# Kernel optimization log

Measured on AMD Instinct MI355X. Metric: run time of the kernel, lower is better.

Reference implementation:

```python
import jax, jax.numpy as jnp
import numpy as np

B, N = 4096, 512


def setup_inputs() -> dict:
    key = jax.random.key(0)
    ks = jax.random.split(key, 8)
    waypoints = jax.random.normal(ks[0], (B, N, 2), dtype=jnp.float32)
    # learned params: scalar smooth_weight + curvature_net MLP (4->64->32->1)
    smooth_weight = jnp.float32(0.3)
    W1 = jax.random.normal(ks[1], (4, 64), dtype=jnp.float32) * 0.5
    b1 = jnp.zeros((64,), dtype=jnp.float32)
    W2 = jax.random.normal(ks[2], (64, 32), dtype=jnp.float32) * 0.125
    b2 = jnp.zeros((32,), dtype=jnp.float32)
    W3 = jax.random.normal(ks[3], (32, 1), dtype=jnp.float32) * 0.18
    b3 = jnp.zeros((1,), dtype=jnp.float32)
    return {"waypoints": waypoints, "smooth_weight": smooth_weight,
            "W1": W1, "b1": b1, "W2": W2, "b2": b2, "W3": W3, "b3": b3}


def _forward(waypoints, smooth_weight, W1, b1, W2, b2, W3, b3):
    Bq, Nq, _ = waypoints.shape
    # finite differences
    d1 = waypoints[:, 1:] - waypoints[:, :-1]          # (B, N-1, 2)
    d2 = d1[:, 1:] - d1[:, :-1]                        # (B, N-2, 2)
    d1 = jnp.concatenate([d1, d1[:, -1:]], axis=1)     # (B, N, 2)
    z = jnp.zeros((Bq, 1, 2), dtype=waypoints.dtype)
    d2 = jnp.concatenate([z, d2, z], axis=1)           # (B, N, 2)
    feats = jnp.concatenate([d1, d2], axis=-1)         # (B, N, 4)
    # curvature MLP -> sigmoid weight in (0,1)
    h = jax.nn.relu(jnp.einsum('bnf,fh->bnh', feats, W1) + b1)
    h = jax.nn.relu(jnp.einsum('bnh,hk->bnk', h, W2) + b2)
    cw = jax.nn.sigmoid(jnp.einsum('bnk,ko->bno', h, W3) + b3)  # (B, N, 1)
    sw = jax.nn.sigmoid(smooth_weight)
    w = sw * (1.0 - cw[..., 0])                        # (B, N)
    # linear recurrence: y_i = w_i * y_{i-1} + (1-w_i) * x_i, y_0 = x_0
    a = jnp.swapaxes(w[:, 1:], 0, 1)                   # (N-1, B)
    x = jnp.swapaxes(waypoints[:, 1:], 0, 1)           # (N-1, B, 2)

    def step(carry, inp):
        a_i, x_i = inp
        y = a_i[:, None] * carry + (1.0 - a_i)[:, None] * x_i
        return y, y

    _, ys = jax.lax.scan(step, waypoints[:, 0], (a, x))
    smoothed = jnp.concatenate([waypoints[:, :1], jnp.swapaxes(ys, 0, 1)], axis=1)
    # endpoints pinned to original (start already equals input)
    smoothed = smoothed.at[:, -1].set(waypoints[:, -1])
    return smoothed


def reference(waypoints, smooth_weight, W1, b1, W2, b2, W3, b3):
    return _forward(waypoints, smooth_weight, W1, b1, W2, b2, W3, b3)
```

## Files before the change

kernel.cpp:

```cpp
#include <hip/hip_runtime.h>
#include <math.h>

#define NPT 512
#define BROWS 4096
#define TAB_U4 17

typedef _Float16 half8 __attribute__((ext_vector_type(8)));
typedef _Float16 h2    __attribute__((ext_vector_type(2)));
typedef float    f32x4 __attribute__((ext_vector_type(4)));
typedef unsigned int u32x4 __attribute__((ext_vector_type(4)));

__device__ __forceinline__ float sigmoidf_fast(float x) {
    return 1.0f / (1.0f + __expf(-x));
}

__device__ __forceinline__ h2 pkrtz(float a, float b) {
    return __builtin_bit_cast(h2, __builtin_amdgcn_cvt_pkrtz(a, b));
}

#if __has_builtin(__builtin_amdgcn_fdot2)
__device__ __forceinline__ float fdot2(h2 a, h2 b, float c) {
    return __builtin_amdgcn_fdot2(__builtin_bit_cast(__fp16 __attribute__((ext_vector_type(2))), a),
                                  __builtin_bit_cast(__fp16 __attribute__((ext_vector_type(2))), b),
                                  c, false);
}
#else
__device__ __forceinline__ float fdot2(h2 a, h2 b, float c) {
    c = fmaf((float)a[0], (float)b[0], c);
    c = fmaf((float)a[1], (float)b[1], c);
    return c;
}
#endif

__global__ __launch_bounds__(64) void setup_kernel(
    const float* __restrict__ W1, const float* __restrict__ b1,
    const float* __restrict__ W2, const float* __restrict__ b2,
    const float* __restrict__ W3, u32x4* __restrict__ tab)
{
    const int lane = threadIdx.x & 63;
    const int nn   = lane & 15;
    const int kg   = lane >> 4;
    const int kg8  = kg * 8;

    half8 Wf00, Wf01, Wf10, Wf11;
    #pragma unroll
    for (int j = 0; j < 8; ++j) {
        Wf00[j] = (_Float16)W2[(0  + kg8 + j) * 32 + 0  + nn];
        Wf01[j] = (_Float16)W2[(0  + kg8 + j) * 32 + 16 + nn];
        Wf10[j] = (_Float16)W2[(32 + kg8 + j) * 32 + 0  + nn];
        Wf11[j] = (_Float16)W2[(32 + kg8 + j) * 32 + 16 + nn];
    }
    tab[0 * 64 + lane] = __builtin_bit_cast(u32x4, Wf00);
    tab[1 * 64 + lane] = __builtin_bit_cast(u32x4, Wf01);
    tab[2 * 64 + lane] = __builtin_bit_cast(u32x4, Wf10);
    tab[3 * 64 + lane] = __builtin_bit_cast(u32x4, Wf11);

    unsigned int wbuf[32], bbuf[8];
    #pragma unroll
    for (int i = 0; i < 8; ++i) {
        const int ch = (i < 4) ? (kg8 + 2 * i) : (32 + kg8 + 2 * (i - 4));
        #pragma unroll
        for (int k = 0; k < 4; ++k) {
            h2 v; v[0] = (_Float16)W1[k * 64 + ch]; v[1] = (_Float16)W1[k * 64 + ch + 1];
            wbuf[k * 8 + i] = __builtin_bit_cast(unsigned int, v);
        }
        h2 bv; bv[0] = (_Float16)b1[ch]; bv[1] = (_Float16)b1[ch + 1];
        bbuf[i] = __builtin_bit_cast(unsigned int, bv);
    }
    #pragma unroll
    for (int p = 0; p < 8; ++p) {
        u32x4 v;
        v[0] = wbuf[p * 4 + 0]; v[1] = wbuf[p * 4 + 1];
        v[2] = wbuf[p * 4 + 2]; v[3] = wbuf[p * 4 + 3];
        tab[(4 + p) * 64 + lane] = v;
    }
    {
        u32x4 v0, v1;
        #pragma unroll
        for (int e = 0; e < 4; ++e) { v0[e] = bbuf[e]; v1[e] = bbuf[4 + e]; }
        tab[12 * 64 + lane] = v0;
        tab[13 * 64 + lane] = v1;
    }
    f32x4 ai0, ai1;
    u32x4 w3v;
    #pragma unroll
    for (int q = 0; q < 4; ++q) {
        const int ch = kg * 4 + q;
        ai0[q] = b2[ch];
        ai1[q] = b2[16 + ch];
    }
    #pragma unroll
    for (int e = 0; e < 2; ++e) {
        h2 a, b;
        a[0] = (_Float16)W3[kg * 4 + 2 * e];
        a[1] = (_Float16)W3[kg * 4 + 2 * e + 1];
        b[0] = (_Float16)W3[16 + kg * 4 + 2 * e];
        b[1] = (_Float16)W3[16 + kg * 4 + 2 * e + 1];
        w3v[e]     = __builtin_bit_cast(unsigned int, a);
        w3v[2 + e] = __builtin_bit_cast(unsigned int, b);
    }
    tab[14 * 64 + lane] = __builtin_bit_cast(u32x4, ai0);
    tab[15 * 64 + lane] = __builtin_bit_cast(u32x4, ai1);
    tab[16 * 64 + lane] = w3v;
}

__global__ __launch_bounds__(256, 4) void wps_kernel(
    const float* __restrict__ wp,
    const float* __restrict__ sww,
    const float* __restrict__ b3,
    const u32x4* __restrict__ tab,
    float* __restrict__ out)
{
    __shared__ float sLg[2][NPT];
    __shared__ float2 sY[2];

    const int t    = threadIdx.x;
    const int lane = t & 63;
    const int wv   = t >> 6;
    const int row0 = blockIdx.x * 2;

    const int nn = lane & 15;
    const int kg = lane >> 4;

    const half8 Wf00 = __builtin_bit_cast(half8, tab[0 * 64 + lane]);
    const half8 Wf01 = __builtin_bit_cast(half8, tab[1 * 64 + lane]);
    const half8 Wf10 = __builtin_bit_cast(half8, tab[2 * 64 + lane]);
    const half8 Wf11 = __builtin_bit_cast(half8, tab[3 * 64 + lane]);

    h2 w1pk[4][8];
    #pragma unroll
    for (int p = 0; p < 8; ++p) {
        u32x4 v = tab[(4 + p) * 64 + lane];
        #pragma unroll
        for (int e = 0; e < 4; ++e) {
            const int j = p * 4 + e;
            w1pk[j >> 3][j & 7] = __builtin_bit_cast(h2, (unsigned int)v[e]);
        }
    }
    h2 b1pk[8];
    {
        u32x4 v0 = tab[12 * 64 + lane];
        u32x4 v1 = tab[13 * 64 + lane];
        #pragma unroll
        for (int e = 0; e < 4; ++e) {
            b1pk[e]     = __builtin_bit_cast(h2, (unsigned int)v0[e]);
            b1pk[4 + e] = __builtin_bit_cast(h2, (unsigned int)v1[e]);
        }
    }
    const f32x4 accInit0 = __builtin_bit_cast(f32x4, tab[14 * 64 + lane]);
    const f32x4 accInit1 = __builtin_bit_cast(f32x4, tab[15 * 64 + lane]);
    h2 w3p[4];
    {
        u32x4 v = tab[16 * 64 + lane];
        #pragma unroll
        for (int e = 0; e < 4; ++e)
            w3p[e] = __builtin_bit_cast(h2, (unsigned int)v[e]);
    }

    const int seg = wv * 128;

    #pragma unroll
    for (int r = 0; r < 2; ++r) {
        const float2* P = (const float2*)(wp + (size_t)(row0 + r) * NPT * 2);

        #pragma unroll
        for (int s = 0; s < 2; ++s) {
            const int base = seg + s * 64;
            const int g    = base + lane;

            float2 p  = P[g];
            float2 pm = P[(g > 0) ? g - 1 : 0];
            float2 pp = P[(g < NPT - 1) ? g + 1 : NPT - 1];
            float d1x, d1y;
            if (g < NPT - 1) { d1x = pp.x - p.x; d1y = pp.y - p.y; }
            else             { d1x = p.x - pm.x; d1y = p.y - pm.y; }
            float d2x = 0.f, d2y = 0.f;
            if (g >= 1 && g <= NPT - 2) {
                d2x = pp.x - 2.f * p.x + pm.x;
                d2y = pp.y - 2.f * p.y + pm.y;
            }
            h2 f01 = pkrtz(d1x, d1y);
            h2 f23 = pkrtz(d2x, d2y);
            const int u01 = __builtin_bit_cast(int, f01);
            const int u23 = __builtin_bit_cast(int, f23);

            float vkeep = 0.f;

            #pragma unroll
            for (int q = 0; q < 4; ++q) {
                h2 r01 = __builtin_bit_cast(h2, __shfl(u01, q * 16 + nn));
                h2 r23 = __builtin_bit_cast(h2, __shfl(u23, q * 16 + nn));
                h2 f0; f0[0] = f0[1] = r01[0];
                h2 f1; f1[0] = f1[1] = r01[1];
                h2 f2; f2[0] = f2[1] = r23[0];
                h2 f3; f3[0] = f3[1] = r23[1];

                union { half8 v; h2 p[4]; } H0, H1;
                #pragma unroll
                for (int i = 0; i < 8; ++i) {
                    h2 h = b1pk[i];
                    h += f0 * w1pk[0][i];
                    h += f1 * w1pk[1][i];
                    h += f2 * w1pk[2][i];
                    h += f3 * w1pk[3][i];
                    h2 z; z[0] = (_Float16)0.f; z[1] = (_Float16)0.f;
                    h = __builtin_elementwise_max(h, z);
                    if (i < 4) H0.p[i] = h; else H1.p[i - 4] = h;
                }

                f32x4 acc0 = accInit0;
                f32x4 acc1 = accInit1;
                acc0 = __builtin_amdgcn_mfma_f32_16x16x32_f16(Wf00, H0.v, acc0, 0, 0, 0);
                acc0 = __builtin_amdgcn_mfma_f32_16x16x32_f16(Wf10, H1.v, acc0, 0, 0, 0);
                acc1 = __builtin_amdgcn_mfma_f32_16x16x32_f16(Wf01, H0.v, acc1, 0, 0, 0);
                acc1 = __builtin_amdgcn_mfma_f32_16x16x32_f16(Wf11, H1.v, acc1, 0, 0, 0);

                h2 zz; zz[0] = (_Float16)0.f; zz[1] = (_Float16)0.f;
                h2 p0 = __builtin_elementwise_max(pkrtz(acc0[0], acc0[1]), zz);
                h2 p1 = __builtin_elementwise_max(pkrtz(acc0[2], acc0[3]), zz);
                h2 p2 = __builtin_elementwise_max(pkrtz(acc1[0], acc1[1]), zz);
                h2 p3 = __builtin_elementwise_max(pkrtz(acc1[2], acc1[3]), zz);
                float v = fdot2(p0, w3p[0], 0.f);
                v = fdot2(p1, w3p[1], v);
                v = fdot2(p2, w3p[2], v);
                v = fdot2(p3, w3p[3], v);
                v += __shfl_xor(v, 16);
                v += __shfl_xor(v, 32);
                vkeep = (q == kg) ? v : vkeep;
            }

            sLg[r][g] = vkeep;
        }
    }

    __syncthreads();

    {
        const int rloc = wv >> 1;
        const int half = wv & 1;
        const int row  = row0 + rloc;
        const float2* P = (const float2*)(wp + (size_t)row * NPT * 2);
        const float bias3 = b3[0];
        const float swv   = sigmoidf_fast(sww[0]);

        const int base = half * 256 + lane * 4;
        float wr[4];
        *reinterpret_cast<float4*>(&wr[0]) =
            *reinterpret_cast<const float4*>(&sLg[rloc][base]);

        const float4* P4 = (const float4*)P;
        float2 pts[4];
        #pragma unroll
        for (int s = 0; s < 2; ++s) {
            float4 v = P4[base / 2 + s];
            pts[2 * s].x     = v.x; pts[2 * s].y     = v.y;
            pts[2 * s + 1].x = v.z; pts[2 * s + 1].y = v.w;
        }

        float a4[4], cx4[4], cy4[4];
        float A = 1.f, Cx = 0.f, Cy = 0.f;
        #pragma unroll
        for (int i = 0; i < 4; ++i) {
            const int g = base + i;
            float a = (g == 0) ? 0.f
                               : swv * (1.f - sigmoidf_fast(wr[i] + bias3));
            float cx = (1.f - a) * pts[i].x;
            float cy = (1.f - a) * pts[i].y;
            a4[i] = a; cx4[i] = cx; cy4[i] = cy;
            Cx = fmaf(a, Cx, cx);
            Cy = fmaf(a, Cy, cy);
            A *= a;
        }
        #pragma unroll
        for (int d = 1; d < 64; d <<= 1) {
            float Ap  = __shfl_up(A, d);
            float Cpx = __shfl_up(Cx, d);
            float Cpy = __shfl_up(Cy, d);
            if (lane >= d) {
                Cx = fmaf(A, Cpx, Cx);
                Cy = fmaf(A, Cpy, Cy);
                A *= Ap;
            }
        }
        float Aex  = __shfl_up(A, 1);
        float Cxex = __shfl_up(Cx, 1);
        float Cyex = __shfl_up(Cy, 1);

        float4* orow = (float4*)(out + (size_t)row * NPT * 2);

        if (half == 0) {
            float yx = (lane == 0) ? 0.f : Cxex;
            float yy = (lane == 0) ? 0.f : Cyex;
            float ox[4], oy[4];
            #pragma unroll
            for (int i = 0; i < 4; ++i) {
                yx = fmaf(a4[i], yx, cx4[i]);
                yy = fmaf(a4[i], yy, cy4[i]);
                ox[i] = yx; oy[i] = yy;
            }
            orow[base / 2]     = make_float4(ox[0], oy[0], ox[1], oy[1]);
            orow[base / 2 + 1] = make_float4(ox[2], oy[2], ox[3], oy[3]);
            if (lane == 63) { sY[rloc].x = yx; sY[rloc].y = yy; }
        }

        __syncthreads();

        if (half == 1) {
            const float2 y255 = sY[rloc];
            float yx = (lane == 0) ? y255.x : fmaf(Aex, y255.x, Cxex);
            float yy = (lane == 0) ? y255.y : fmaf(Aex, y255.y, Cyex);
            float ox[4], oy[4];
            #pragma unroll
            for (int i = 0; i < 4; ++i) {
                yx = fmaf(a4[i], yx, cx4[i]);
                yy = fmaf(a4[i], yy, cy4[i]);
                ox[i] = yx; oy[i] = yy;
            }
            if (lane == 63) {
                float2 pe = P[NPT - 1];
                ox[3] = pe.x; oy[3] = pe.y;
            }
            orow[base / 2]     = make_float4(ox[0], oy[0], ox[1], oy[1]);
            orow[base / 2 + 1] = make_float4(ox[2], oy[2], ox[3], oy[3]);
        }
    }
}

extern "C" void kernel_launch(void* const* d_in, const int* in_sizes, int n_in,
                              void* d_out, int out_size, void* d_ws, size_t ws_size,
                              hipStream_t stream) {
    const float* wp  = (const float*)d_in[0];
    const float* sww = (const float*)d_in[1];
    const float* W1  = (const float*)d_in[2];
    const float* b1  = (const float*)d_in[3];
    const float* W2  = (const float*)d_in[4];
    const float* b2  = (const float*)d_in[5];
    const float* W3  = (const float*)d_in[6];
    const float* b3  = (const float*)d_in[7];
    float* out = (float*)d_out;
    u32x4* tab = (u32x4*)d_ws;

    setup_kernel<<<1, 64, 0, stream>>>(W1, b1, W2, b2, W3, tab);
    wps_kernel<<<BROWS / 2, 256, 0, stream>>>(wp, sww, b3, tab, out);
}
```

Before: 33.18 us.

## Compute first MLP layer with MFMA instead of packed-half VALU

Moves the 4->64 first layer (with bias folded in through a ones row) from packed fp16 VALU FMAs onto 16x16x16 MFMA instructions. The second layer is restructured into eight 16x16x16 MFMAs whose output layout feeds directly from layer one, so no cross-lane shuffle is needed between layers, and the weight table shrinks from 17 to 9 entries. This trades VALU work and per-lane weight registers for more MFMA issues and extra fmax/convert work on the layer-one outputs, and most of the padded K dimension of layer one is zeros.

```diff
diff --git a/kernel.cpp b/kernel.cpp
--- a/kernel.cpp
+++ b/kernel.cpp
@@ -3,9 +3,10 @@
 
 #define NPT 512
 #define BROWS 4096
-#define TAB_U4 17
+#define TAB_U4 9
 
 typedef _Float16 half8 __attribute__((ext_vector_type(8)));
+typedef _Float16 half4 __attribute__((ext_vector_type(4)));
 typedef _Float16 h2    __attribute__((ext_vector_type(2)));
 typedef float    f32x4 __attribute__((ext_vector_type(4)));
 typedef unsigned int u32x4 __attribute__((ext_vector_type(4)));
@@ -31,6 +32,22 @@
     return c;
 }
 #endif
+
+#if __has_builtin(__builtin_amdgcn_mfma_f32_16x16x16f16)
+__device__ __forceinline__ f32x4 mfma16(half4 a, half4 b, f32x4 c) {
+    return __builtin_amdgcn_mfma_f32_16x16x16f16(a, b, c, 0, 0, 0);
+}
+#else
+__device__ __forceinline__ f32x4 mfma16(half4 a, half4 b, f32x4 c) {
+    half8 a8 = {a[0], a[1], a[2], a[3],
+                (_Float16)0.f, (_Float16)0.f, (_Float16)0.f, (_Float16)0.f};
+    half8 b8 = {b[0], b[1], b[2], b[3],
+                (_Float16)0.f, (_Float16)0.f, (_Float16)0.f, (_Float16)0.f};
+    return __builtin_amdgcn_mfma_f32_16x16x32_f16(a8, b8, c, 0, 0, 0);
+}
+#endif
+
+union H4 { half4 v; h2 p[2]; unsigned int w[2]; };
 
 __global__ __launch_bounds__(64) void setup_kernel(
     const float* __restrict__ W1, const float* __restrict__ b1,
@@ -40,55 +57,63 @@
     const int lane = threadIdx.x & 63;
     const int nn   = lane & 15;
     const int kg   = lane >> 4;
-    const int kg8  = kg * 8;
-
-    half8 Wf00, Wf01, Wf10, Wf11;
-    #pragma unroll
-    for (int j = 0; j < 8; ++j) {
-        Wf00[j] = (_Float16)W2[(0  + kg8 + j) * 32 + 0  + nn];
-        Wf01[j] = (_Float16)W2[(0  + kg8 + j) * 32 + 16 + nn];
-        Wf10[j] = (_Float16)W2[(32 + kg8 + j) * 32 + 0  + nn];
-        Wf11[j] = (_Float16)W2[(32 + kg8 + j) * 32 + 16 + nn];
-    }
-    tab[0 * 64 + lane] = __builtin_bit_cast(u32x4, Wf00);
-    tab[1 * 64 + lane] = __builtin_bit_cast(u32x4, Wf01);
-    tab[2 * 64 + lane] = __builtin_bit_cast(u32x4, Wf10);
-    tab[3 * 64 + lane] = __builtin_bit_cast(u32x4, Wf11);
-
-    unsigned int wbuf[32], bbuf[8];
-    #pragma unroll
-    for (int i = 0; i < 8; ++i) {
-        const int ch = (i < 4) ? (kg8 + 2 * i) : (32 + kg8 + 2 * (i - 4));
-        #pragma unroll
-        for (int k = 0; k < 4; ++k) {
-            h2 v; v[0] = (_Float16)W1[k * 64 + ch]; v[1] = (_Float16)W1[k * 64 + ch + 1];
-            wbuf[k * 8 + i] = __builtin_bit_cast(unsigned int, v);
-        }
-        h2 bv; bv[0] = (_Float16)b1[ch]; bv[1] = (_Float16)b1[ch + 1];
-        bbuf[i] = __builtin_bit_cast(unsigned int, bv);
-    }
-    #pragma unroll
-    for (int p = 0; p < 8; ++p) {
-        u32x4 v;
-        v[0] = wbuf[p * 4 + 0]; v[1] = wbuf[p * 4 + 1];
-        v[2] = wbuf[p * 4 + 2]; v[3] = wbuf[p * 4 + 3];
-        tab[(4 + p) * 64 + lane] = v;
+
+    unsigned int a1w[8];
+    #pragma unroll
+    for (int t = 0; t < 4; ++t) {
+        const int ch = t * 16 + nn;
+        h2 j01, j23;
+        j01[0] = (_Float16)0.f; j01[1] = (_Float16)0.f;
+        j23[0] = (_Float16)0.f; j23[1] = (_Float16)0.f;
+        if (kg == 0) {
+            j01[0] = (_Float16)W1[0 * 64 + ch]; j01[1] = (_Float16)W1[1 * 64 + ch];
+            j23[0] = (_Float16)W1[2 * 64 + ch]; j23[1] = (_Float16)W1[3 * 64 + ch];
+        } else if (kg == 1) {
+            j01[0] = (_Float16)b1[ch];
+        }
+        a1w[t * 2 + 0] = __builtin_bit_cast(unsigned int, j01);
+        a1w[t * 2 + 1] = __builtin_bit_cast(unsigned int, j23);
     }
     {
         u32x4 v0, v1;
         #pragma unroll
-        for (int e = 0; e < 4; ++e) { v0[e] = bbuf[e]; v1[e] = bbuf[4 + e]; }
-        tab[12 * 64 + lane] = v0;
-        tab[13 * 64 + lane] = v1;
-    }
+        for (int e = 0; e < 4; ++e) { v0[e] = a1w[e]; v1[e] = a1w[4 + e]; }
+        tab[0 * 64 + lane] = v0;
+        tab[1 * 64 + lane] = v1;
+    }
+
+    #pragma unroll
+    for (int m = 0; m < 2; ++m) {
+        unsigned int a2w[8];
+        #pragma unroll
+        for (int s = 0; s < 4; ++s) {
+            const int bc  = s * 16 + kg * 4;
+            const int col = m * 16 + nn;
+            h2 j01, j23;
+            j01[0] = (_Float16)W2[(bc + 0) * 32 + col];
+            j01[1] = (_Float16)W2[(bc + 1) * 32 + col];
+            j23[0] = (_Float16)W2[(bc + 2) * 32 + col];
+            j23[1] = (_Float16)W2[(bc + 3) * 32 + col];
+            a2w[s * 2 + 0] = __builtin_bit_cast(unsigned int, j01);
+            a2w[s * 2 + 1] = __builtin_bit_cast(unsigned int, j23);
+        }
+        u32x4 v0, v1;
+        #pragma unroll
+        for (int e = 0; e < 4; ++e) { v0[e] = a2w[e]; v1[e] = a2w[4 + e]; }
+        tab[(2 + m * 2) * 64 + lane] = v0;
+        tab[(3 + m * 2) * 64 + lane] = v1;
+    }
+
     f32x4 ai0, ai1;
+    #pragma unroll
+    for (int r = 0; r < 4; ++r) {
+        ai0[r] = b2[kg * 4 + r];
+        ai1[r] = b2[16 + kg * 4 + r];
+    }
+    tab[6 * 64 + lane] = __builtin_bit_cast(u32x4, ai0);
+    tab[7 * 64 + lane] = __builtin_bit_cast(u32x4, ai1);
+
     u32x4 w3v;
-    #pragma unroll
-    for (int q = 0; q < 4; ++q) {
-        const int ch = kg * 4 + q;
-        ai0[q] = b2[ch];
-        ai1[q] = b2[16 + ch];
-    }
     #pragma unroll
     for (int e = 0; e < 2; ++e) {
         h2 a, b;
@@ -99,9 +124,7 @@
         w3v[e]     = __builtin_bit_cast(unsigned int, a);
         w3v[2 + e] = __builtin_bit_cast(unsigned int, b);
     }
-    tab[14 * 64 + lane] = __builtin_bit_cast(u32x4, ai0);
-    tab[15 * 64 + lane] = __builtin_bit_cast(u32x4, ai1);
-    tab[16 * 64 + lane] = w3v;
+    tab[8 * 64 + lane] = w3v;
 }
 
 __global__ __launch_bounds__(256, 4) void wps_kernel(
@@ -122,40 +145,43 @@
     const int nn = lane & 15;
     const int kg = lane >> 4;
 
-    const half8 Wf00 = __builtin_bit_cast(half8, tab[0 * 64 + lane]);
-    const half8 Wf01 = __builtin_bit_cast(half8, tab[1 * 64 + lane]);
-    const half8 Wf10 = __builtin_bit_cast(half8, tab[2 * 64 + lane]);
-    const half8 Wf11 = __builtin_bit_cast(half8, tab[3 * 64 + lane]);
-
-    h2 w1pk[4][8];
-    #pragma unroll
-    for (int p = 0; p < 8; ++p) {
-        u32x4 v = tab[(4 + p) * 64 + lane];
-        #pragma unroll
-        for (int e = 0; e < 4; ++e) {
-            const int j = p * 4 + e;
-            w1pk[j >> 3][j & 7] = __builtin_bit_cast(h2, (unsigned int)v[e]);
-        }
-    }
-    h2 b1pk[8];
-    {
-        u32x4 v0 = tab[12 * 64 + lane];
-        u32x4 v1 = tab[13 * 64 + lane];
-        #pragma unroll
-        for (int e = 0; e < 4; ++e) {
-            b1pk[e]     = __builtin_bit_cast(h2, (unsigned int)v0[e]);
-            b1pk[4 + e] = __builtin_bit_cast(h2, (unsigned int)v1[e]);
-        }
-    }
-    const f32x4 accInit0 = __builtin_bit_cast(f32x4, tab[14 * 64 + lane]);
-    const f32x4 accInit1 = __builtin_bit_cast(f32x4, tab[15 * 64 + lane]);
+    H4 A1[4];
+    {
+        u32x4 v0 = tab[0 * 64 + lane];
+        u32x4 v1 = tab[1 * 64 + lane];
+        A1[0].w[0] = v0[0]; A1[0].w[1] = v0[1];
+        A1[1].w[0] = v0[2]; A1[1].w[1] = v0[3];
+        A1[2].w[0] = v1[0]; A1[2].w[1] = v1[1];
+        A1[3].w[0] = v1[2]; A1[3].w[1] = v1[3];
+    }
+    H4 A2m0[4], A2m1[4];
+    {
+        u32x4 v0 = tab[2 * 64 + lane];
+        u32x4 v1 = tab[3 * 64 + lane];
+        u32x4 v2 = tab[4 * 64 + lane];
+        u32x4 v3 = tab[5 * 64 + lane];
+        A2m0[0].w[0] = v0[0]; A2m0[0].w[1] = v0[1];
+        A2m0[1].w[0] = v0[2]; A2m0[1].w[1] = v0[3];
+        A2m0[2].w[0] = v1[0]; A2m0[2].w[1] = v1[1];
+        A2m0[3].w[0] = v1[2]; A2m0[3].w[1] = v1[3];
+        A2m1[0].w[0] = v2[0]; A2m1[0].w[1] = v2[1];
+        A2m1[1].w[0] = v2[2]; A2m1[1].w[1] = v2[3];
+        A2m1[2].w[0] = v3[0]; A2m1[2].w[1] = v3[1];
+        A2m1[3].w[0] = v3[2]; A2m1[3].w[1] = v3[3];
+    }
+    const f32x4 accInit0 = __builtin_bit_cast(f32x4, tab[6 * 64 + lane]);
+    const f32x4 accInit1 = __builtin_bit_cast(f32x4, tab[7 * 64 + lane]);
     h2 w3p[4];
     {
-        u32x4 v = tab[16 * 64 + lane];
+        u32x4 v = tab[8 * 64 + lane];
         #pragma unroll
         for (int e = 0; e < 4; ++e)
             w3p[e] = __builtin_bit_cast(h2, (unsigned int)v[e]);
     }
+
+    h2 zeroh; zeroh[0] = (_Float16)0.f; zeroh[1] = (_Float16)0.f;
+    h2 one0;  one0[0]  = (_Float16)1.f; one0[1]  = (_Float16)0.f;
+    const f32x4 zero4 = {0.f, 0.f, 0.f, 0.f};
 
     const int seg = wv * 128;
 
@@ -190,36 +216,41 @@
             for (int q = 0; q < 4; ++q) {
                 h2 r01 = __builtin_bit_cast(h2, __shfl(u01, q * 16 + nn));
                 h2 r23 = __builtin_bit_cast(h2, __shfl(u23, q * 16 + nn));
-                h2 f0; f0[0] = f0[1] = r01[0];
-                h2 f1; f1[0] = f1[1] = r01[1];
-                h2 f2; f2[0] = f2[1] = r23[0];
-                h2 f3; f3[0] = f3[1] = r23[1];
-
-                union { half8 v; h2 p[4]; } H0, H1;
-                #pragma unroll
-                for (int i = 0; i < 8; ++i) {
-                    h2 h = b1pk[i];
-                    h += f0 * w1pk[0][i];
-                    h += f1 * w1pk[1][i];
-                    h += f2 * w1pk[2][i];
-                    h += f3 * w1pk[3][i];
-                    h2 z; z[0] = (_Float16)0.f; z[1] = (_Float16)0.f;
-                    h = __builtin_elementwise_max(h, z);
-                    if (i < 4) H0.p[i] = h; else H1.p[i - 4] = h;
-                }
+
+                H4 B1;
+                B1.p[0] = (kg == 0) ? r01 : ((kg == 1) ? one0 : zeroh);
+                B1.p[1] = (kg == 0) ? r23 : zeroh;
+
+                f32x4 d0 = mfma16(A1[0].v, B1.v, zero4);
+                f32x4 d1 = mfma16(A1[1].v, B1.v, zero4);
+                f32x4 d2 = mfma16(A1[2].v, B1.v, zero4);
+                f32x4 d3 = mfma16(A1[3].v, B1.v, zero4);
+
+                H4 B2[4];
+                B2[0].p[0] = pkrtz(fmaxf(d0[0], 0.f), fmaxf(d0[1], 0.f));
+                B2[0].p[1] = pkrtz(fmaxf(d0[2], 0.f), fmaxf(d0[3], 0.f));
+                B2[1].p[0] = pkrtz(fmaxf(d1[0], 0.f), fmaxf(d1[1], 0.f));
+                B2[1].p[1] = pkrtz(fmaxf(d1[2], 0.f), fmaxf(d1[3], 0.f));
+                B2[2].p[0] = pkrtz(fmaxf(d2[0], 0.f), fmaxf(d2[1], 0.f));
+                B2[2].p[1] = pkrtz(fmaxf(d2[2], 0.f), fmaxf(d2[3], 0.f));
+                B2[3].p[0] = pkrtz(fmaxf(d3[0], 0.f), fmaxf(d3[1], 0.f));
+                B2[3].p[1] = pkrtz(fmaxf(d3[2], 0.f), fmaxf(d3[3], 0.f));
 
                 f32x4 acc0 = accInit0;
                 f32x4 acc1 = accInit1;
-                acc0 = __builtin_amdgcn_mfma_f32_16x16x32_f16(Wf00, H0.v, acc0, 0, 0, 0);
-                acc0 = __builtin_amdgcn_mfma_f32_16x16x32_f16(Wf10, H1.v, acc0, 0, 0, 0);
-                acc1 = __builtin_amdgcn_mfma_f32_16x16x32_f16(Wf01, H0.v, acc1, 0, 0, 0);
-                acc1 = __builtin_amdgcn_mfma_f32_16x16x32_f16(Wf11, H1.v, acc1, 0, 0, 0);
-
-                h2 zz; zz[0] = (_Float16)0.f; zz[1] = (_Float16)0.f;
-                h2 p0 = __builtin_elementwise_max(pkrtz(acc0[0], acc0[1]), zz);
-                h2 p1 = __builtin_elementwise_max(pkrtz(acc0[2], acc0[3]), zz);
-                h2 p2 = __builtin_elementwise_max(pkrtz(acc1[0], acc1[1]), zz);
-                h2 p3 = __builtin_elementwise_max(pkrtz(acc1[2], acc1[3]), zz);
+                acc0 = mfma16(A2m0[0].v, B2[0].v, acc0);
+                acc1 = mfma16(A2m1[0].v, B2[0].v, acc1);
+                acc0 = mfma16(A2m0[1].v, B2[1].v, acc0);
+                acc1 = mfma16(A2m1[1].v, B2[1].v, acc1);
+                acc0 = mfma16(A2m0[2].v, B2[2].v, acc0);
+                acc1 = mfma16(A2m1[2].v, B2[2].v, acc1);
+                acc0 = mfma16(A2m0[3].v, B2[3].v, acc0);
+                acc1 = mfma16(A2m1[3].v, B2[3].v, acc1);
+
+                h2 p0 = __builtin_elementwise_max(pkrtz(acc0[0], acc0[1]), zeroh);
+                h2 p1 = __builtin_elementwise_max(pkrtz(acc0[2], acc0[3]), zeroh);
+                h2 p2 = __builtin_elementwise_max(pkrtz(acc1[0], acc1[1]), zeroh);
+                h2 p3 = __builtin_elementwise_max(pkrtz(acc1[2], acc1[3]), zeroh);
                 float v = fdot2(p0, w3p[0], 0.f);
                 v = fdot2(p1, w3p[1], v);
                 v = fdot2(p2, w3p[2], v);
```

New measurement: 35.51 us. 7.0% more time.

## Move first MLP layer onto 32x32 MFMA and chain layers via permlane swaps

Applied to the files above, without the earlier changes.

The first layer (4->64 with bias) now runs as two 32x32x16 MFMAs, with the bias folded in through a constant-one input column, replacing packed-half VALU FMAs. Its output is repacked in registers with v_permlane32_swap to form the B operand of four 32x32x16 MFMAs for the second layer, so no extra shuffles are needed. Each wave now processes 32 points per MFMA group instead of looping four times over 16. The weight table shrinks, and launch bounds are raised to 5 blocks per CU for occupancy. The change depends on the gfx950 permlane32_swap instruction, and the b2 bias is now added in half precision after rounding.

```diff
diff --git a/kernel.cpp b/kernel.cpp
--- a/kernel.cpp
+++ b/kernel.cpp
@@ -3,11 +3,11 @@
 
 #define NPT 512
 #define BROWS 4096
-#define TAB_U4 17
-
-typedef _Float16 half8 __attribute__((ext_vector_type(8)));
-typedef _Float16 h2    __attribute__((ext_vector_type(2)));
-typedef float    f32x4 __attribute__((ext_vector_type(4)));
+#define TAB_U4 10
+
+typedef _Float16 half8  __attribute__((ext_vector_type(8)));
+typedef _Float16 h2     __attribute__((ext_vector_type(2)));
+typedef float    f32x16 __attribute__((ext_vector_type(16)));
 typedef unsigned int u32x4 __attribute__((ext_vector_type(4)));
 
 __device__ __forceinline__ float sigmoidf_fast(float x) {
@@ -31,6 +31,24 @@
     return c;
 }
 #endif
+
+union H8 { half8 v; h2 p[4]; unsigned int w[4]; };
+
+__device__ __forceinline__ f32x16 mfma32(half8 a, half8 b, f32x16 c) {
+    return __builtin_amdgcn_mfma_f32_32x32x16_f16(a, b, c, 0, 0, 0);
+}
+
+__device__ __forceinline__ void pl32swap(unsigned &a, unsigned &b) {
+    asm volatile("v_permlane32_swap_b32 %0, %1" : "+v"(a), "+v"(b));
+}
+
+__device__ __forceinline__ half8 makeB2(unsigned p0, unsigned p1,
+                                        unsigned p2, unsigned p3) {
+    pl32swap(p0, p2);
+    pl32swap(p1, p3);
+    H8 B; B.w[0] = p0; B.w[1] = p1; B.w[2] = p2; B.w[3] = p3;
+    return B.v;
+}
 
 __global__ __launch_bounds__(64) void setup_kernel(
     const float* __restrict__ W1, const float* __restrict__ b1,
@@ -38,73 +56,62 @@
     const float* __restrict__ W3, u32x4* __restrict__ tab)
 {
     const int lane = threadIdx.x & 63;
-    const int nn   = lane & 15;
-    const int kg   = lane >> 4;
-    const int kg8  = kg * 8;
-
-    half8 Wf00, Wf01, Wf10, Wf11;
-    #pragma unroll
-    for (int j = 0; j < 8; ++j) {
-        Wf00[j] = (_Float16)W2[(0  + kg8 + j) * 32 + 0  + nn];
-        Wf01[j] = (_Float16)W2[(0  + kg8 + j) * 32 + 16 + nn];
-        Wf10[j] = (_Float16)W2[(32 + kg8 + j) * 32 + 0  + nn];
-        Wf11[j] = (_Float16)W2[(32 + kg8 + j) * 32 + 16 + nn];
-    }
-    tab[0 * 64 + lane] = __builtin_bit_cast(u32x4, Wf00);
-    tab[1 * 64 + lane] = __builtin_bit_cast(u32x4, Wf01);
-    tab[2 * 64 + lane] = __builtin_bit_cast(u32x4, Wf10);
-    tab[3 * 64 + lane] = __builtin_bit_cast(u32x4, Wf11);
-
-    unsigned int wbuf[32], bbuf[8];
-    #pragma unroll
-    for (int i = 0; i < 8; ++i) {
-        const int ch = (i < 4) ? (kg8 + 2 * i) : (32 + kg8 + 2 * (i - 4));
-        #pragma unroll
-        for (int k = 0; k < 4; ++k) {
-            h2 v; v[0] = (_Float16)W1[k * 64 + ch]; v[1] = (_Float16)W1[k * 64 + ch + 1];
-            wbuf[k * 8 + i] = __builtin_bit_cast(unsigned int, v);
-        }
-        h2 bv; bv[0] = (_Float16)b1[ch]; bv[1] = (_Float16)b1[ch + 1];
-        bbuf[i] = __builtin_bit_cast(unsigned int, bv);
-    }
-    #pragma unroll
-    for (int p = 0; p < 8; ++p) {
-        u32x4 v;
-        v[0] = wbuf[p * 4 + 0]; v[1] = wbuf[p * 4 + 1];
-        v[2] = wbuf[p * 4 + 2]; v[3] = wbuf[p * 4 + 3];
-        tab[(4 + p) * 64 + lane] = v;
+    const int c    = lane & 31;
+    const int hi   = lane >> 5;
+
+    #pragma unroll
+    for (int t = 0; t < 2; ++t) {
+        H8 a;
+        a.w[0] = 0u; a.w[1] = 0u; a.w[2] = 0u; a.w[3] = 0u;
+        if (hi == 0) {
+            const int ch = t * 32 + c;
+            h2 v0; v0[0] = (_Float16)W1[0 * 64 + ch]; v0[1] = (_Float16)W1[1 * 64 + ch];
+            h2 v1; v1[0] = (_Float16)W1[2 * 64 + ch]; v1[1] = (_Float16)W1[3 * 64 + ch];
+            h2 v2; v2[0] = (_Float16)b1[ch];          v2[1] = (_Float16)0.f;
+            a.p[0] = v0; a.p[1] = v1; a.p[2] = v2;
+        }
+        u32x4 o; o[0] = a.w[0]; o[1] = a.w[1]; o[2] = a.w[2]; o[3] = a.w[3];
+        tab[t * 64 + lane] = o;
+    }
+
+    #pragma unroll
+    for (int s = 0; s < 4; ++s) {
+        H8 a;
+        #pragma unroll
+        for (int jj = 0; jj < 4; ++jj) {
+            const int k = s * 16 + hi * 8 + 2 * jj;
+            h2 v; v[0] = (_Float16)W2[k * 32 + c]; v[1] = (_Float16)W2[(k + 1) * 32 + c];
+            a.p[jj] = v;
+        }
+        u32x4 o; o[0] = a.w[0]; o[1] = a.w[1]; o[2] = a.w[2]; o[3] = a.w[3];
+        tab[(2 + s) * 64 + lane] = o;
+    }
+
+    unsigned bw[8], ww[8];
+    #pragma unroll
+    for (int rr = 0; rr < 8; ++rr) {
+        const int q   = 2 * rr;
+        const int row = (q & 3) + 8 * (q >> 2) + 4 * hi;
+        h2 bv; bv[0] = (_Float16)b2[row]; bv[1] = (_Float16)b2[row + 1];
+        h2 wv; wv[0] = (_Float16)W3[row]; wv[1] = (_Float16)W3[row + 1];
+        bw[rr] = __builtin_bit_cast(unsigned, bv);
+        ww[rr] = __builtin_bit_cast(unsigned, wv);
     }
     {
-        u32x4 v0, v1;
-        #pragma unroll
-        for (int e = 0; e < 4; ++e) { v0[e] = bbuf[e]; v1[e] = bbuf[4 + e]; }
-        tab[12 * 64 + lane] = v0;
-        tab[13 * 64 + lane] = v1;
-    }
-    f32x4 ai0, ai1;
-    u32x4 w3v;
-    #pragma unroll
-    for (int q = 0; q < 4; ++q) {
-        const int ch = kg * 4 + q;
-        ai0[q] = b2[ch];
-        ai1[q] = b2[16 + ch];
-    }
-    #pragma unroll
-    for (int e = 0; e < 2; ++e) {
-        h2 a, b;
-        a[0] = (_Float16)W3[kg * 4 + 2 * e];
-        a[1] = (_Float16)W3[kg * 4 + 2 * e + 1];
-        b[0] = (_Float16)W3[16 + kg * 4 + 2 * e];
-        b[1] = (_Float16)W3[16 + kg * 4 + 2 * e + 1];
-        w3v[e]     = __builtin_bit_cast(unsigned int, a);
-        w3v[2 + e] = __builtin_bit_cast(unsigned int, b);
-    }
-    tab[14 * 64 + lane] = __builtin_bit_cast(u32x4, ai0);
-    tab[15 * 64 + lane] = __builtin_bit_cast(u32x4, ai1);
-    tab[16 * 64 + lane] = w3v;
-}
-
-__global__ __launch_bounds__(256, 4) void wps_kernel(
+        u32x4 o0, o1, o2, o3;
+        #pragma unroll
+        for (int e = 0; e < 4; ++e) {
+            o0[e] = bw[e]; o1[e] = bw[4 + e];
+            o2[e] = ww[e]; o3[e] = ww[4 + e];
+        }
+        tab[6 * 64 + lane] = o0;
+        tab[7 * 64 + lane] = o1;
+        tab[8 * 64 + lane] = o2;
+        tab[9 * 64 + lane] = o3;
+    }
+}
+
+__global__ __launch_bounds__(256, 5) void wps_kernel(
     const float* __restrict__ wp,
     const float* __restrict__ sww,
     const float* __restrict__ b3,
@@ -118,44 +125,40 @@
     const int lane = t & 63;
     const int wv   = t >> 6;
     const int row0 = blockIdx.x * 2;
-
-    const int nn = lane & 15;
-    const int kg = lane >> 4;
-
-    const half8 Wf00 = __builtin_bit_cast(half8, tab[0 * 64 + lane]);
-    const half8 Wf01 = __builtin_bit_cast(half8, tab[1 * 64 + lane]);
-    const half8 Wf10 = __builtin_bit_cast(half8, tab[2 * 64 + lane]);
-    const half8 Wf11 = __builtin_bit_cast(half8, tab[3 * 64 + lane]);
-
-    h2 w1pk[4][8];
-    #pragma unroll
-    for (int p = 0; p < 8; ++p) {
-        u32x4 v = tab[(4 + p) * 64 + lane];
+    const int c    = lane & 31;
+
+    half8 A1t[2];
+    #pragma unroll
+    for (int i = 0; i < 2; ++i) {
+        u32x4 v = tab[i * 64 + lane];
+        H8 a; a.w[0] = v[0]; a.w[1] = v[1]; a.w[2] = v[2]; a.w[3] = v[3];
+        A1t[i] = a.v;
+    }
+    half8 A2s[4];
+    #pragma unroll
+    for (int i = 0; i < 4; ++i) {
+        u32x4 v = tab[(2 + i) * 64 + lane];
+        H8 a; a.w[0] = v[0]; a.w[1] = v[1]; a.w[2] = v[2]; a.w[3] = v[3];
+        A2s[i] = a.v;
+    }
+    h2 b2p[8], w3p[8];
+    {
+        u32x4 v0 = tab[6 * 64 + lane];
+        u32x4 v1 = tab[7 * 64 + lane];
+        u32x4 v2 = tab[8 * 64 + lane];
+        u32x4 v3 = tab[9 * 64 + lane];
         #pragma unroll
         for (int e = 0; e < 4; ++e) {
-            const int j = p * 4 + e;
-            w1pk[j >> 3][j & 7] = __builtin_bit_cast(h2, (unsigned int)v[e]);
-        }
-    }
-    h2 b1pk[8];
-    {
-        u32x4 v0 = tab[12 * 64 + lane];
-        u32x4 v1 = tab[13 * 64 + lane];
-        #pragma unroll
-        for (int e = 0; e < 4; ++e) {
-            b1pk[e]     = __builtin_bit_cast(h2, (unsigned int)v0[e]);
-            b1pk[4 + e] = __builtin_bit_cast(h2, (unsigned int)v1[e]);
-        }
-    }
-    const f32x4 accInit0 = __builtin_bit_cast(f32x4, tab[14 * 64 + lane]);
-    const f32x4 accInit1 = __builtin_bit_cast(f32x4, tab[15 * 64 + lane]);
-    h2 w3p[4];
-    {
-        u32x4 v = tab[16 * 64 + lane];
-        #pragma unroll
-        for (int e = 0; e < 4; ++e)
-            w3p[e] = __builtin_bit_cast(h2, (unsigned int)v[e]);
-    }
+            b2p[e]     = __builtin_bit_cast(h2, (unsigned)v0[e]);
+            b2p[4 + e] = __builtin_bit_cast(h2, (unsigned)v1[e]);
+            w3p[e]     = __builtin_bit_cast(h2, (unsigned)v2[e]);
+            w3p[4 + e] = __builtin_bit_cast(h2, (unsigned)v3[e]);
+        }
+    }
+
+    h2 zeroh; zeroh[0] = (_Float16)0.f; zeroh[1] = (_Float16)0.f;
+    const f32x16 zero16 = {0.f,0.f,0.f,0.f,0.f,0.f,0.f,0.f,
+                           0.f,0.f,0.f,0.f,0.f,0.f,0.f,0.f};
 
     const int seg = wv * 128;
 
@@ -164,8 +167,8 @@
         const float2* P = (const float2*)(wp + (size_t)(row0 + r) * NPT * 2);
 
         #pragma unroll
-        for (int s = 0; s < 2; ++s) {
-            const int base = seg + s * 64;
+        for (int s2 = 0; s2 < 2; ++s2) {
+            const int base = seg + s2 * 64;
             const int g    = base + lane;
 
             float2 p  = P[g];
@@ -179,57 +182,46 @@
                 d2x = pp.x - 2.f * p.x + pm.x;
                 d2y = pp.y - 2.f * p.y + pm.y;
             }
-            h2 f01 = pkrtz(d1x, d1y);
-            h2 f23 = pkrtz(d2x, d2y);
-            const int u01 = __builtin_bit_cast(int, f01);
-            const int u23 = __builtin_bit_cast(int, f23);
-
-            float vkeep = 0.f;
+            const int u01 = __builtin_bit_cast(int, pkrtz(d1x, d1y));
+            const int u23 = __builtin_bit_cast(int, pkrtz(d2x, d2y));
 
             #pragma unroll
-            for (int q = 0; q < 4; ++q) {
-                h2 r01 = __builtin_bit_cast(h2, __shfl(u01, q * 16 + nn));
-                h2 r23 = __builtin_bit_cast(h2, __shfl(u23, q * 16 + nn));
-                h2 f0; f0[0] = f0[1] = r01[0];
-                h2 f1; f1[0] = f1[1] = r01[1];
-                h2 f2; f2[0] = f2[1] = r23[0];
-                h2 f3; f3[0] = f3[1] = r23[1];
-
-                union { half8 v; h2 p[4]; } H0, H1;
+            for (int T = 0; T < 2; ++T) {
+                const unsigned r01 = (unsigned)__shfl(u01, T * 32 + c);
+                const unsigned r23 = (unsigned)__shfl(u23, T * 32 + c);
+                H8 B1;
+                B1.w[0] = r01; B1.w[1] = r23;
+                B1.w[2] = 0x00003C00u; B1.w[3] = 0u;
+
+                f32x16 pre0 = mfma32(A1t[0], B1.v, zero16);
+                f32x16 pre1 = mfma32(A1t[1], B1.v, zero16);
+
+                unsigned pw0[8], pw1[8];
                 #pragma unroll
-                for (int i = 0; i < 8; ++i) {
-                    h2 h = b1pk[i];
-                    h += f0 * w1pk[0][i];
-                    h += f1 * w1pk[1][i];
-                    h += f2 * w1pk[2][i];
-                    h += f3 * w1pk[3][i];
-                    h2 z; z[0] = (_Float16)0.f; z[1] = (_Float16)0.f;
-                    h = __builtin_elementwise_max(h, z);
-                    if (i < 4) H0.p[i] = h; else H1.p[i - 4] = h;
+                for (int rr = 0; rr < 8; ++rr) {
+                    pw0[rr] = __builtin_bit_cast(unsigned,
+                        __builtin_elementwise_max(pkrtz(pre0[2*rr], pre0[2*rr+1]), zeroh));
+                    pw1[rr] = __builtin_bit_cast(unsigned,
+                        __builtin_elementwise_max(pkrtz(pre1[2*rr], pre1[2*rr+1]), zeroh));
                 }
 
-                f32x4 acc0 = accInit0;
-                f32x4 acc1 = accInit1;
-                acc0 = __builtin_amdgcn_mfma_f32_16x16x32_f16(Wf00, H0.v, acc0, 0, 0, 0);
-                acc0 = __builtin_amdgcn_mfma_f32_16x16x32_f16(Wf10, H1.v, acc0, 0, 0, 0);
-                acc1 = __builtin_amdgcn_mfma_f32_16x16x32_f16(Wf01, H0.v, acc1, 0, 0, 0);
-                acc1 = __builtin_amdgcn_mfma_f32_16x16x32_f16(Wf11, H1.v, acc1, 0, 0, 0);
-
-                h2 zz; zz[0] = (_Float16)0.f; zz[1] = (_Float16)0.f;
-                h2 p0 = __builtin_elementwise_max(pkrtz(acc0[0], acc0[1]), zz);
-                h2 p1 = __builtin_elementwise_max(pkrtz(acc0[2], acc0[3]), zz);
-                h2 p2 = __builtin_elementwise_max(pkrtz(acc1[0], acc1[1]), zz);
-                h2 p3 = __builtin_elementwise_max(pkrtz(acc1[2], acc1[3]), zz);
-                float v = fdot2(p0, w3p[0], 0.f);
-                v = fdot2(p1, w3p[1], v);
-                v = fdot2(p2, w3p[2], v);
-                v = fdot2(p3, w3p[3], v);
-                v += __shfl_xor(v, 16);
+                f32x16 acc = zero16;
+                acc = mfma32(A2s[0], makeB2(pw0[0], pw0[1], pw0[2], pw0[3]), acc);
+                acc = mfma32(A2s[1], makeB2(pw0[4], pw0[5], pw0[6], pw0[7]), acc);
+                acc = mfma32(A2s[2], makeB2(pw1[0], pw1[1], pw1[2], pw1[3]), acc);
+                acc = mfma32(A2s[3], makeB2(pw1[4], pw1[5], pw1[6], pw1[7]), acc);
+
+                float v = 0.f;
+                #pragma unroll
+                for (int rr = 0; rr < 8; ++rr) {
+                    h2 tt = pkrtz(acc[2*rr], acc[2*rr+1]);
+                    tt = tt + b2p[rr];
+                    tt = __builtin_elementwise_max(tt, zeroh);
+                    v = fdot2(tt, w3p[rr], v);
+                }
                 v += __shfl_xor(v, 32);
-                vkeep = (q == kg) ? v : vkeep;
-            }
-
-            sLg[r][g] = vkeep;
+                if (lane < 32) sLg[r][base + T * 32 + lane] = v;
+            }
         }
     }
 
```

New measurement: 31.47 us. 1.05x faster.
